# Performance work log

Measured on AMD Instinct MI355X. Metric: run time of the kernel, lower is better.

## Reference

```python
import jax, jax.numpy as jnp
import numpy as np

N, K = 65536, 128  # rays, samples per ray


def setup_inputs() -> dict:
    key = jax.random.key(0)
    k1, k2 = jax.random.split(key)
    densities = jax.random.uniform(k1, (N, K, 1), dtype=jnp.float32)
    deltas = jax.random.uniform(k2, (N, K, 1), dtype=jnp.float32)
    return {"densities": densities, "deltas": deltas}


def reference(densities, deltas):
    # delta_density: [N, K, 1]
    delta_density = deltas * densities
    alphas = 1.0 - jnp.exp(-delta_density)
    # exclusive cumulative optical depth along the sample axis (dim -2)
    acc = jnp.cumsum(delta_density[..., :-1, :], axis=-2)  # [N, K-1, 1]
    acc = jnp.concatenate(
        [jnp.zeros((delta_density.shape[0], 1, 1), dtype=delta_density.dtype), acc],
        axis=-2,
    )  # [N, K, 1]
    transmittance = jnp.exp(-acc)
    weights = alphas * transmittance
    return weights, transmittance
```

## Files before the change

kernel.cpp:

```cpp
#include <hip/hip_runtime.h>


__global__ __launch_bounds__(256) void RaySamples_34454227648765_kernel(
    const float* __restrict__ dens, const float* __restrict__ delt,
    float* __restrict__ outw, float* __restrict__ outT, int n4)
{
    int i = blockIdx.x * blockDim.x + threadIdx.x;
    if (i >= n4) return;

    const float4 d  = reinterpret_cast<const float4*>(dens)[i];
    const float4 dl = reinterpret_cast<const float4*>(delt)[i];

    float dd0 = d.x * dl.x;
    float dd1 = d.y * dl.y;
    float dd2 = d.z * dl.z;
    float dd3 = d.w * dl.w;

    float s = dd0 + dd1 + dd2 + dd3;

    int lane = threadIdx.x & 31;
    float inc = s;
    #pragma unroll
    for (int off = 1; off < 32; off <<= 1) {
        float v = __shfl_up(inc, off, 32);
        inc += (lane >= off) ? v : 0.0f;
    }
    float a0 = inc - s;
    float a1 = a0 + dd0;
    float a2 = a1 + dd1;
    float a3 = a2 + dd2;
    float a4 = a3 + dd3;

    float t0 = __expf(-a0);
    float t1 = __expf(-a1);
    float t2 = __expf(-a2);
    float t3 = __expf(-a3);
    float t4 = __expf(-a4);

    float4 T = make_float4(t0, t1, t2, t3);
    float4 W = make_float4(t0 - t1, t1 - t2, t2 - t3, t3 - t4);

    reinterpret_cast<float4*>(outw)[i] = W;
    reinterpret_cast<float4*>(outT)[i] = T;
}

extern "C" void kernel_launch(void* const* d_in, const int* in_sizes, int n_in,
                              void* d_out, int out_size, void* d_ws, size_t ws_size,
                              hipStream_t stream) {
    const float* dens = (const float*)d_in[0];
    const float* delt = (const float*)d_in[1];
    float* out = (float*)d_out;

    const int NK = in_sizes[0];
    const int n4 = NK / 4;
    float* outw = out;
    float* outT = out + NK;

    const int block = 256;
    const int grid = (n4 + block - 1) / block;
    RaySamples_34454227648765_kernel<<<grid, block, 0, stream>>>(
        dens, delt, outw, outT, n4);
}
```

Before: 112.0 us.

## Process two float4 chunks per thread with nontemporal loads and stores

Halves the grid so each thread handles two independent float4 segments, at i0 and i0+stride, interleaving their shuffle scans to raise memory-level parallelism. All global loads and stores become nontemporal to avoid polluting cache on this streaming workload. The work is unchanged, but register use per thread roughly doubles. A scalar tail path covers an odd leftover segment.

Result: slower. 120.7 us (+7.7%).

```diff
diff --git a/kernel.cpp b/kernel.cpp
--- a/kernel.cpp
+++ b/kernel.cpp
@@ -1,47 +1,86 @@
 #include <hip/hip_runtime.h>
 
+
+typedef float f4 __attribute__((ext_vector_type(4)));
 
 __global__ __launch_bounds__(256) void RaySamples_34454227648765_kernel(
     const float* __restrict__ dens, const float* __restrict__ delt,
     float* __restrict__ outw, float* __restrict__ outT, int n4)
 {
-    int i = blockIdx.x * blockDim.x + threadIdx.x;
-    if (i >= n4) return;
+    const int stride = gridDim.x * blockDim.x;
+    const int i0 = blockIdx.x * blockDim.x + threadIdx.x;
+    const int i1 = i0 + stride;
+    const int lane = threadIdx.x & 31;
 
-    const float4 d  = reinterpret_cast<const float4*>(dens)[i];
-    const float4 dl = reinterpret_cast<const float4*>(delt)[i];
+    const f4* __restrict__ d4 = reinterpret_cast<const f4*>(dens);
+    const f4* __restrict__ l4 = reinterpret_cast<const f4*>(delt);
+    f4* __restrict__ w4 = reinterpret_cast<f4*>(outw);
+    f4* __restrict__ t4 = reinterpret_cast<f4*>(outT);
 
-    float dd0 = d.x * dl.x;
-    float dd1 = d.y * dl.y;
-    float dd2 = d.z * dl.z;
-    float dd3 = d.w * dl.w;
+    if (i1 < n4) {
+        const f4 dA = __builtin_nontemporal_load(d4 + i0);
+        const f4 lA = __builtin_nontemporal_load(l4 + i0);
+        const f4 dB = __builtin_nontemporal_load(d4 + i1);
+        const f4 lB = __builtin_nontemporal_load(l4 + i1);
 
-    float s = dd0 + dd1 + dd2 + dd3;
+        float A0 = dA.x * lA.x, A1 = dA.y * lA.y,
+              A2 = dA.z * lA.z, A3 = dA.w * lA.w;
+        float B0 = dB.x * lB.x, B1 = dB.y * lB.y,
+              B2 = dB.z * lB.z, B3 = dB.w * lB.w;
 
-    int lane = threadIdx.x & 31;
-    float inc = s;
-    #pragma unroll
-    for (int off = 1; off < 32; off <<= 1) {
-        float v = __shfl_up(inc, off, 32);
-        inc += (lane >= off) ? v : 0.0f;
+        float sA = A0 + A1 + A2 + A3;
+        float sB = B0 + B1 + B2 + B3;
+
+        float incA = sA, incB = sB;
+        #pragma unroll
+        for (int off = 1; off < 32; off <<= 1) {
+            float vA = __shfl_up(incA, off, 32);
+            float vB = __shfl_up(incB, off, 32);
+            incA += (lane >= off) ? vA : 0.0f;
+            incB += (lane >= off) ? vB : 0.0f;
+        }
+
+        float aA0 = incA - sA;
+        float aA1 = aA0 + A0, aA2 = aA1 + A1, aA3 = aA2 + A2, aA4 = aA3 + A3;
+        float aB0 = incB - sB;
+        float aB1 = aB0 + B0, aB2 = aB1 + B1, aB3 = aB2 + B2, aB4 = aB3 + B3;
+
+        float tA0 = __expf(-aA0), tA1 = __expf(-aA1), tA2 = __expf(-aA2),
+              tA3 = __expf(-aA3), tA4 = __expf(-aA4);
+        float tB0 = __expf(-aB0), tB1 = __expf(-aB1), tB2 = __expf(-aB2),
+              tB3 = __expf(-aB3), tB4 = __expf(-aB4);
+
+        f4 WA; WA.x = tA0 - tA1; WA.y = tA1 - tA2; WA.z = tA2 - tA3; WA.w = tA3 - tA4;
+        f4 TA; TA.x = tA0; TA.y = tA1; TA.z = tA2; TA.w = tA3;
+        f4 WB; WB.x = tB0 - tB1; WB.y = tB1 - tB2; WB.z = tB2 - tB3; WB.w = tB3 - tB4;
+        f4 TB; TB.x = tB0; TB.y = tB1; TB.z = tB2; TB.w = tB3;
+
+        __builtin_nontemporal_store(WA, w4 + i0);
+        __builtin_nontemporal_store(TA, t4 + i0);
+        __builtin_nontemporal_store(WB, w4 + i1);
+        __builtin_nontemporal_store(TB, t4 + i1);
+    } else if (i0 < n4) {
+        const f4 d  = __builtin_nontemporal_load(d4 + i0);
+        const f4 dl = __builtin_nontemporal_load(l4 + i0);
+
+        float dd0 = d.x * dl.x, dd1 = d.y * dl.y,
+              dd2 = d.z * dl.z, dd3 = d.w * dl.w;
+        float s = dd0 + dd1 + dd2 + dd3;
+        float inc = s;
+        #pragma unroll
+        for (int off = 1; off < 32; off <<= 1) {
+            float v = __shfl_up(inc, off, 32);
+            inc += (lane >= off) ? v : 0.0f;
+        }
+        float a0 = inc - s;
+        float a1 = a0 + dd0, a2 = a1 + dd1, a3 = a2 + dd2, a4 = a3 + dd3;
+        float t0 = __expf(-a0), t1 = __expf(-a1), t2 = __expf(-a2),
+              t3 = __expf(-a3), t4v = __expf(-a4);
+        f4 W; W.x = t0 - t1; W.y = t1 - t2; W.z = t2 - t3; W.w = t3 - t4v;
+        f4 T; T.x = t0; T.y = t1; T.z = t2; T.w = t3;
+        __builtin_nontemporal_store(W, w4 + i0);
+        __builtin_nontemporal_store(T, t4 + i0);
     }
-    float a0 = inc - s;
-    float a1 = a0 + dd0;
-    float a2 = a1 + dd1;
-    float a3 = a2 + dd2;
-    float a4 = a3 + dd3;
-
-    float t0 = __expf(-a0);
-    float t1 = __expf(-a1);
-    float t2 = __expf(-a2);
-    float t3 = __expf(-a3);
-    float t4 = __expf(-a4);
-
-    float4 T = make_float4(t0, t1, t2, t3);
-    float4 W = make_float4(t0 - t1, t1 - t2, t2 - t3, t3 - t4);
-
-    reinterpret_cast<float4*>(outw)[i] = W;
-    reinterpret_cast<float4*>(outT)[i] = T;
 }
 
 extern "C" void kernel_launch(void* const* d_in, const int* in_sizes, int n_in,
@@ -57,7 +96,8 @@
     float* outT = out + NK;
 
     const int block = 256;
-    const int grid = (n4 + block - 1) / block;
+    const int threads_needed = (n4 + 1) / 2;
+    const int grid = (threads_needed + block - 1) / block;
     RaySamples_34454227648765_kernel<<<grid, block, 0, stream>>>(
         dens, delt, outw, outT, n4);
 }
```
